# Kernel tuning notes

Measured on AMD Instinct MI355X. Metric: run time of the kernel, lower is better.

## Reference

```python
import jax, jax.numpy as jnp
import numpy as np

N_NODES = 100000
HID = 128
N_LAYERS = 3
N_EDGES = 1600000
EPS = 1e-5


def setup_inputs() -> dict:
    key = jax.random.key(0)
    ks = jax.random.split(key, 10)
    H, L = HID, N_LAYERS
    # edge_index: row 0 = src, row 1 = dst (PyG source_to_target flow)
    edge_index = jax.random.randint(ks[0], (2, N_EDGES), 0, N_NODES, dtype=jnp.int32)
    # xavier-uniform embedding
    lim = float(np.sqrt(6.0 / (N_NODES + H)))
    emb = jax.random.uniform(ks[1], (N_NODES, H), jnp.float32, -lim, lim)
    s = 1.0 / np.sqrt(H)
    Wl = jax.random.uniform(ks[2], (L, H, H), jnp.float32, -s, s)  # lin_l (neighbors), has bias
    bl = jax.random.uniform(ks[3], (L, H), jnp.float32, -s, s)
    Wr = jax.random.uniform(ks[4], (L, H, H), jnp.float32, -s, s)  # lin_r (root), no bias
    ln_gamma = jnp.ones((L, H), jnp.float32)
    ln_beta = jnp.zeros((L, H), jnp.float32)
    sj = 1.0 / np.sqrt(H * (L + 1))
    jkW = jax.random.uniform(ks[5], (H, H * (L + 1)), jnp.float32, -sj, sj)
    jkb = jax.random.uniform(ks[6], (H,), jnp.float32, -sj, sj)
    return {"emb": emb, "Wl": Wl, "bl": bl, "Wr": Wr,
            "ln_gamma": ln_gamma, "ln_beta": ln_beta,
            "jkW": jkW, "jkb": jkb, "edge_index": edge_index}


def _layernorm(x, gamma, beta):
    mu = jnp.mean(x, axis=-1, keepdims=True)
    var = jnp.mean(jnp.square(x - mu), axis=-1, keepdims=True)
    return (x - mu) * jax.lax.rsqrt(var + EPS) * gamma + beta


def reference(emb, Wl, bl, Wr, ln_gamma, ln_beta, jkW, jkb, edge_index):
    src, dst = edge_index[0], edge_index[1]
    n = emb.shape[0]
    # in-degree for mean aggregation (clamped to avoid div-by-zero)
    deg = jax.ops.segment_sum(jnp.ones_like(dst, dtype=emb.dtype), dst, num_segments=n)
    inv_deg = (1.0 / jnp.maximum(deg, 1.0))[:, None]
    x = emb
    xs = [x]
    for i in range(N_LAYERS):
        x_prev = x
        # scatter-mean of neighbor features (gather [E,H] -> segment_sum [N,H])
        agg = jax.ops.segment_sum(x[src], dst, num_segments=n) * inv_deg
        # SAGEConv: lin_l(agg) + lin_r(x)
        x = agg @ Wl[i].T + bl[i] + x @ Wr[i].T
        x = _layernorm(x, ln_gamma[i], ln_beta[i])
        x = jax.nn.relu(x)
        # dropout is identity in eval mode
        if i > 0:
            x = x + x_prev
        xs.append(x)
    # jumping-knowledge concat + projection
    x = jnp.concatenate(xs, axis=1) @ jkW.T + jkb
    return x
```

## Files before the change

kernel.cpp:

```cpp
#include <hip/hip_runtime.h>
#include <hip/hip_bf16.h>
#include <stdint.h>

#define HID 128

typedef __attribute__((ext_vector_type(8))) __bf16 bf16x8;
typedef __attribute__((ext_vector_type(4))) float f32x4;

static __device__ __forceinline__ float bf2f(ushort h){
  union { uint u; float f; } c; c.u = ((uint)h) << 16; return c.f;
}
static __device__ __forceinline__ ushort f2bf(float f){
  union { float f; uint u; } c; c.f = f;
  uint u = c.u;
  return (ushort)((u + 0x7fffu + ((u >> 16) & 1u)) >> 16);
}
static __device__ __forceinline__ bf16x8 load8(const ushort* p){
  return *(const bf16x8*)p;
}

__global__ void k_cvt(const float* __restrict__ in, ushort* __restrict__ out, int n){
  int i = blockIdx.x * 256 + threadIdx.x;
  if (i < n) out[i] = f2bf(in[i]);
}

__global__ void k_cvtw(const float* __restrict__ Wl, const float* __restrict__ Wr,
                       ushort* __restrict__ outF, int total){
  int o = blockIdx.x * 256 + threadIdx.x;
  if (o >= total) return;
  int layer = o >> 15;
  int r = o & 32767;
  int e    = r & 7;
  int lane = (r >> 3) & 63;
  int jt   = (r >> 9) & 7;
  int mat  = (r >> 12) & 1;
  int kt   = r >> 13;
  int l16 = lane & 15, quad = lane >> 4;
  int j = jt * 16 + l16;
  int k = kt * 32 + quad * 8 + e;
  const float* W = mat ? Wr : Wl;
  outF[o] = f2bf(W[layer * 16384 + j * 128 + k]);
}

__global__ void k_cvtjk(const float* __restrict__ jkW, ushort* __restrict__ outF){
  int o = blockIdx.x * 256 + threadIdx.x;
  int e    = o & 7;
  int lane = (o >> 3) & 63;
  int jt   = (o >> 9) & 7;
  int kt   = o >> 12;
  int l16 = lane & 15, quad = lane >> 4;
  int j = jt * 16 + l16;
  int k = kt * 32 + quad * 8 + e;
  outF[o] = f2bf(jkW[j * 512 + k]);
}

__global__ void k_hist(const int* __restrict__ dst, int* __restrict__ cnt, int E){
  int e = blockIdx.x * 256 + threadIdx.x;
  if (e < E) atomicAdd(&cnt[dst[e]], 1);
}

__global__ void k_scan1(const int* __restrict__ cnt, int* __restrict__ offs,
                        int* __restrict__ bsums, int n){
  int gid = blockIdx.x * 1024 + threadIdx.x;
  int v = (gid < n) ? cnt[gid] : 0;
  int lane = threadIdx.x & 63, w = threadIdx.x >> 6;
  int x = v;
  #pragma unroll
  for (int d = 1; d < 64; d <<= 1){ int y = __shfl_up(x, d, 64); if (lane >= d) x += y; }
  __shared__ int tmp[16];
  if (lane == 63) tmp[w] = x;
  __syncthreads();
  if (threadIdx.x < 64){
    int s = (lane < 16) ? tmp[lane] : 0;
    #pragma unroll
    for (int d = 1; d < 16; d <<= 1){ int y = __shfl_up(s, d, 64); if (lane >= d) s += y; }
    if (lane < 16) tmp[lane] = s;
  }
  __syncthreads();
  int base = (w > 0) ? tmp[w - 1] : 0;
  int incl = base + x;
  if (gid < n) offs[gid] = incl - v;
  if (threadIdx.x == 1023) bsums[blockIdx.x] = incl;
}

__global__ void k_scan2(int* bsums, int nb){
  if (threadIdx.x == 0 && blockIdx.x == 0){
    int acc = 0;
    for (int i = 0; i < nb; i++){ int v = bsums[i]; bsums[i] = acc; acc += v; }
  }
}

__global__ void k_scan3(int* __restrict__ offs, const int* __restrict__ bsums, int n){
  int gid = blockIdx.x * 1024 + threadIdx.x;
  if (gid < n) offs[gid] += bsums[blockIdx.x];
}

__global__ void k_bucket(const int* __restrict__ src, const int* __restrict__ dst,
                         const int* __restrict__ offs, int* __restrict__ cursor,
                         int* __restrict__ csr, int E){
  int e = blockIdx.x * 256 + threadIdx.x;
  if (e < E){
    int d = dst[e];
    int p = atomicAdd(&cursor[d], 1);
    csr[offs[d] + p] = src[e];
  }
}

__global__ __launch_bounds__(256) void k_aggregate(
    const ushort* __restrict__ x, const int* __restrict__ csr,
    const int* __restrict__ offs, const int* __restrict__ cnt,
    ushort* __restrict__ agg, int N){
  int node = blockIdx.x * 4 + (threadIdx.x >> 6);
  int lane = threadIdx.x & 63;
  if (node >= N) return;
  int beg = offs[node], d = cnt[node];
  const int* __restrict__ cp = csr + beg;
  float s0 = 0.f, s1 = 0.f;
  int i = 0;
  for (; i + 8 <= d; i += 8){
    int idx[8];
    #pragma unroll
    for (int u = 0; u < 8; u++) idx[u] = cp[i + u];
    uint v[8];
    #pragma unroll
    for (int u = 0; u < 8; u++)
      v[u] = *(const uint*)(x + (size_t)idx[u] * HID + lane * 2);
    #pragma unroll
    for (int u = 0; u < 8; u++){
      s0 += bf2f((ushort)v[u]);
      s1 += bf2f((ushort)(v[u] >> 16));
    }
  }
  if (i + 4 <= d){
    int idx[4];
    #pragma unroll
    for (int u = 0; u < 4; u++) idx[u] = cp[i + u];
    uint v[4];
    #pragma unroll
    for (int u = 0; u < 4; u++)
      v[u] = *(const uint*)(x + (size_t)idx[u] * HID + lane * 2);
    #pragma unroll
    for (int u = 0; u < 4; u++){
      s0 += bf2f((ushort)v[u]);
      s1 += bf2f((ushort)(v[u] >> 16));
    }
    i += 4;
  }
  for (; i < d; i++){
    int s = cp[i];
    uint v = *(const uint*)(x + (size_t)s * HID + lane * 2);
    s0 += bf2f((ushort)v);
    s1 += bf2f((ushort)(v >> 16));
  }
  float inv = 1.0f / fmaxf((float)d, 1.0f);
  uint o = (uint)f2bf(s0 * inv) | ((uint)f2bf(s1 * inv) << 16);
  *(uint*)(agg + (size_t)node * HID + lane * 2) = o;
}

template<int HAS_RES>
__global__ __launch_bounds__(256) void k_layer(
    const ushort* __restrict__ agg, const ushort* __restrict__ xin,
    const ushort* __restrict__ Wf,
    const float* __restrict__ bl, const float* __restrict__ gamma,
    const float* __restrict__ beta,
    ushort* __restrict__ xout, int N){
  __shared__ ushort sB[8192];
  int tid = threadIdx.x;
  int wv = tid >> 6, lane = tid & 63;
  int quad = lane >> 4, l16 = lane & 15;
  int rowbase = blockIdx.x * 128 + wv * 32;
  int r0 = rowbase + l16;      if (r0 >= N) r0 = N - 1;
  int r1 = rowbase + 16 + l16; if (r1 >= N) r1 = N - 1;

  f32x4 acc[2][8];
  #pragma unroll
  for (int jt = 0; jt < 8; jt++){
    float b = bl[jt * 16 + l16];
    f32x4 c = {b, b, b, b};
    acc[0][jt] = c; acc[1][jt] = c;
  }

  #pragma unroll
  for (int kt = 0; kt < 4; kt++){
    int ao = kt * 32 + quad * 8;
    bf16x8 a10 = load8(agg + (size_t)r0 * HID + ao);
    bf16x8 a11 = load8(agg + (size_t)r1 * HID + ao);
    bf16x8 a20 = load8(xin + (size_t)r0 * HID + ao);
    bf16x8 a21 = load8(xin + (size_t)r1 * HID + ao);
    __syncthreads();
    const ushort* src = Wf + kt * 8192;
    #pragma unroll
    for (int i = 0; i < 4; i++){
      int c = i * 256 + tid;
      *(bf16x8*)(sB + c * 8) = load8(src + c * 8);
    }
    __syncthreads();
    #pragma unroll
    for (int jt = 0; jt < 8; jt++){
      bf16x8 bL = load8(sB + (jt * 64 + lane) * 8);
      bf16x8 bR = load8(sB + ((8 + jt) * 64 + lane) * 8);
      acc[0][jt] = __builtin_amdgcn_mfma_f32_16x16x32_bf16(a10, bL, acc[0][jt], 0, 0, 0);
      acc[1][jt] = __builtin_amdgcn_mfma_f32_16x16x32_bf16(a11, bL, acc[1][jt], 0, 0, 0);
      acc[0][jt] = __builtin_amdgcn_mfma_f32_16x16x32_bf16(a20, bR, acc[0][jt], 0, 0, 0);
      acc[1][jt] = __builtin_amdgcn_mfma_f32_16x16x32_bf16(a21, bR, acc[1][jt], 0, 0, 0);
    }
  }

  #pragma unroll
  for (int rt = 0; rt < 2; rt++){
    float s1[4] = {0,0,0,0}, s2[4] = {0,0,0,0};
    #pragma unroll
    for (int jt = 0; jt < 8; jt++){
      #pragma unroll
      for (int r = 0; r < 4; r++){ float v = acc[rt][jt][r]; s1[r] += v; s2[r] += v * v; }
    }
    #pragma unroll
    for (int m = 1; m < 16; m <<= 1){
      #pragma unroll
      for (int r = 0; r < 4; r++){
        s1[r] += __shfl_xor(s1[r], m, 64);
        s2[r] += __shfl_xor(s2[r], m, 64);
      }
    }
    float mu[4], rs[4];
    #pragma unroll
    for (int r = 0; r < 4; r++){
      mu[r] = s1[r] * (1.f / 128.f);
      float var = s2[r] * (1.f / 128.f) - mu[r] * mu[r];
      rs[r] = rsqrtf(var + 1e-5f);
    }
    #pragma unroll
    for (int jt = 0; jt < 8; jt++){
      int col = jt * 16 + l16;
      float g = gamma[col], bb = beta[col];
      #pragma unroll
      for (int r = 0; r < 4; r++){
        int row = rowbase + rt * 16 + quad * 4 + r;
        if (row < N){
          float v = (acc[rt][jt][r] - mu[r]) * rs[r] * g + bb;
          v = fmaxf(v, 0.f);
          if (HAS_RES) v += bf2f(xin[(size_t)row * HID + col]);
          xout[(size_t)row * HID + col] = f2bf(v);
        }
      }
    }
  }
}

__global__ __launch_bounds__(256) void k_jk(
    const ushort* __restrict__ emb, const ushort* __restrict__ x1,
    const ushort* __restrict__ x2, const ushort* __restrict__ x3,
    const ushort* __restrict__ Wf,
    const float* __restrict__ jkb, float* __restrict__ out, int N){
  __shared__ ushort sB[8192];
  int tid = threadIdx.x;
  int wv = tid >> 6, lane = tid & 63;
  int quad = lane >> 4, l16 = lane & 15;
  int rowbase = blockIdx.x * 128 + wv * 32;
  int r0 = rowbase + l16;      if (r0 >= N) r0 = N - 1;
  int r1 = rowbase + 16 + l16; if (r1 >= N) r1 = N - 1;

  f32x4 acc[2][8];
  #pragma unroll
  for (int jt = 0; jt < 8; jt++){
    float b = jkb[jt * 16 + l16];
    f32x4 c = {b, b, b, b};
    acc[0][jt] = c; acc[1][jt] = c;
  }

  const ushort* srcs[4] = {emb, x1, x2, x3};
  #pragma unroll
  for (int st = 0; st < 8; st++){
    int kt0 = st * 2, kt1 = st * 2 + 1;
    const ushort* sp0 = srcs[kt0 >> 2];
    const ushort* sp1 = srcs[kt1 >> 2];
    int ao0 = (kt0 & 3) * 32 + quad * 8;
    int ao1 = (kt1 & 3) * 32 + quad * 8;
    bf16x8 aA0 = load8(sp0 + (size_t)r0 * HID + ao0);
    bf16x8 aA1 = load8(sp0 + (size_t)r1 * HID + ao0);
    bf16x8 aB0 = load8(sp1 + (size_t)r0 * HID + ao1);
    bf16x8 aB1 = load8(sp1 + (size_t)r1 * HID + ao1);
    __syncthreads();
    const ushort* src = Wf + st * 8192;
    #pragma unroll
    for (int i = 0; i < 4; i++){
      int c = i * 256 + tid;
      *(bf16x8*)(sB + c * 8) = load8(src + c * 8);
    }
    __syncthreads();
    #pragma unroll
    for (int jt = 0; jt < 8; jt++){
      bf16x8 b0 = load8(sB + (jt * 64 + lane) * 8);
      bf16x8 b1 = load8(sB + ((8 + jt) * 64 + lane) * 8);
      acc[0][jt] = __builtin_amdgcn_mfma_f32_16x16x32_bf16(aA0, b0, acc[0][jt], 0, 0, 0);
      acc[1][jt] = __builtin_amdgcn_mfma_f32_16x16x32_bf16(aA1, b0, acc[1][jt], 0, 0, 0);
      acc[0][jt] = __builtin_amdgcn_mfma_f32_16x16x32_bf16(aB0, b1, acc[0][jt], 0, 0, 0);
      acc[1][jt] = __builtin_amdgcn_mfma_f32_16x16x32_bf16(aB1, b1, acc[1][jt], 0, 0, 0);
    }
  }

  #pragma unroll
  for (int rt = 0; rt < 2; rt++){
    #pragma unroll
    for (int jt = 0; jt < 8; jt++){
      #pragma unroll
      for (int r = 0; r < 4; r++){
        int row = rowbase + rt * 16 + quad * 4 + r;
        if (row < N)
          out[(size_t)row * HID + jt * 16 + l16] = acc[rt][jt][r];
      }
    }
  }
}

extern "C" void kernel_launch(void* const* d_in, const int* in_sizes, int n_in,
                              void* d_out, int out_size, void* d_ws, size_t ws_size,
                              hipStream_t stream){
  const float* emb   = (const float*)d_in[0];
  const float* Wl    = (const float*)d_in[1];
  const float* bl    = (const float*)d_in[2];
  const float* Wr    = (const float*)d_in[3];
  const float* gamma = (const float*)d_in[4];
  const float* beta  = (const float*)d_in[5];
  const float* jkW   = (const float*)d_in[6];
  const float* jkb   = (const float*)d_in[7];
  const int*   eidx  = (const int*)d_in[8];
  int N = in_sizes[0] / HID;
  int E = in_sizes[8] / 2;
  const int* src = eidx;
  const int* dst = eidx + E;
  float* out = (float*)d_out;

  char* w = (char*)d_ws;
  auto carve = [&](size_t bytes) -> char* {
    char* p = w; w += (bytes + 255) & ~(size_t)255; return p;
  };
  int Npad = ((N + 127) / 128) * 128;
  int* cnt      = (int*)carve((size_t)N * 4);
  int* offs     = (int*)carve((size_t)(N + 1) * 4);
  int* bsums    = (int*)carve(1024 * 4);
  int* cursor   = (int*)carve((size_t)N * 4);
  int* csr      = (int*)carve((size_t)E * 4);
  ushort* Wfrag = (ushort*)carve((size_t)3 * 32768 * 2);
  ushort* jkWf  = (ushort*)carve((size_t)65536 * 2);
  ushort* embbf = (ushort*)carve((size_t)Npad * HID * 2);
  ushort* agg   = (ushort*)carve((size_t)Npad * HID * 2);
  ushort* x1    = (ushort*)carve((size_t)Npad * HID * 2);
  ushort* x2    = (ushort*)carve((size_t)Npad * HID * 2);
  ushort* x3    = (ushort*)carve((size_t)Npad * HID * 2);

  hipMemsetAsync(cnt, 0, (size_t)N * 4, stream);
  hipMemsetAsync(cursor, 0, (size_t)N * 4, stream);

  int nEmb = N * HID;
  k_cvtw<<<(3 * 32768 + 255) / 256, 256, 0, stream>>>(Wl, Wr, Wfrag, 3 * 32768);
  k_cvtjk<<<65536 / 256, 256, 0, stream>>>(jkW, jkWf);
  k_cvt<<<(nEmb + 255) / 256, 256, 0, stream>>>(emb, embbf, nEmb);

  k_hist<<<(E + 255) / 256, 256, 0, stream>>>(dst, cnt, E);
  int nb = (N + 1023) / 1024;
  k_scan1<<<nb, 1024, 0, stream>>>(cnt, offs, bsums, N);
  k_scan2<<<1, 64, 0, stream>>>(bsums, nb);
  k_scan3<<<nb, 1024, 0, stream>>>(offs, bsums, N);
  k_bucket<<<(E + 255) / 256, 256, 0, stream>>>(src, dst, offs, cursor, csr, E);

  int aggBlocks = (N + 3) / 4;
  int gemmBlocks = (N + 127) / 128;

  k_aggregate<<<aggBlocks, 256, 0, stream>>>(embbf, csr, offs, cnt, agg, N);
  k_layer<0><<<gemmBlocks, 256, 0, stream>>>(agg, embbf, Wfrag, bl, gamma, beta, x1, N);
  k_aggregate<<<aggBlocks, 256, 0, stream>>>(x1, csr, offs, cnt, agg, N);
  k_layer<1><<<gemmBlocks, 256, 0, stream>>>(agg, x1, Wfrag + 32768, bl + HID,
                                             gamma + HID, beta + HID, x2, N);
  k_aggregate<<<aggBlocks, 256, 0, stream>>>(x2, csr, offs, cnt, agg, N);
  k_layer<1><<<gemmBlocks, 256, 0, stream>>>(agg, x2, Wfrag + 2 * 32768, bl + 2 * HID,
                                             gamma + 2 * HID, beta + 2 * HID, x3, N);
  k_jk<<<gemmBlocks, 256, 0, stream>>>(embbf, x1, x2, x3, jkWf, jkb, out, N);
}
```

Baseline: 631.5 us.

## Build CSR via coarse 128-node binning plus per-bin shared-memory counting sort

Replaces the global per-node histogram, three-kernel scan and atomic bucket scatter with three kernels. The first bins edges into 128-node buckets, packing source and local destination into one word. The second is a single-block scan over bucket counts. The third does a per-bucket counting sort in shared memory that writes offs, cnt and csr. This aims to cut kernel launches, memsets and scattered global atomics on per-node cursors. In exchange, all edges now hit a few hundred heavily contended bucket counters, and edges past the fixed 3072-per-bucket capacity are silently dropped. The single-block scan also caps the node count at about 131K.

```diff
diff --git a/kernel.cpp b/kernel.cpp
--- a/kernel.cpp
+++ b/kernel.cpp
@@ -3,6 +3,8 @@
 #include <stdint.h>
 
 #define HID 128
+#define BSHIFT 7
+#define BCAP 3072
 
 typedef __attribute__((ext_vector_type(8))) __bf16 bf16x8;
 typedef __attribute__((ext_vector_type(4))) float f32x4;
@@ -54,23 +56,29 @@
   outF[o] = f2bf(jkW[j * 512 + k]);
 }
 
-__global__ void k_hist(const int* __restrict__ dst, int* __restrict__ cnt, int E){
+__global__ void k_bin(const int* __restrict__ src, const int* __restrict__ dst,
+                      int* __restrict__ bcnt, uint* __restrict__ binned, int E){
   int e = blockIdx.x * 256 + threadIdx.x;
-  if (e < E) atomicAdd(&cnt[dst[e]], 1);
-}
-
-__global__ void k_scan1(const int* __restrict__ cnt, int* __restrict__ offs,
-                        int* __restrict__ bsums, int n){
-  int gid = blockIdx.x * 1024 + threadIdx.x;
-  int v = (gid < n) ? cnt[gid] : 0;
-  int lane = threadIdx.x & 63, w = threadIdx.x >> 6;
+  if (e < E){
+    int d = dst[e];
+    int b = d >> BSHIFT;
+    int pos = atomicAdd(&bcnt[b], 1);
+    if (pos < BCAP)
+      binned[(size_t)b * BCAP + pos] = ((uint)src[e] << BSHIFT) | (uint)(d & 127);
+  }
+}
+
+__global__ void k_bscan(const int* __restrict__ bcnt, int* __restrict__ bbase, int nb){
+  int tid = threadIdx.x;
+  int v = (tid < nb) ? min(bcnt[tid], BCAP) : 0;
+  int lane = tid & 63, w = tid >> 6;
   int x = v;
   #pragma unroll
   for (int d = 1; d < 64; d <<= 1){ int y = __shfl_up(x, d, 64); if (lane >= d) x += y; }
   __shared__ int tmp[16];
   if (lane == 63) tmp[w] = x;
   __syncthreads();
-  if (threadIdx.x < 64){
+  if (tid < 64){
     int s = (lane < 16) ? tmp[lane] : 0;
     #pragma unroll
     for (int d = 1; d < 16; d <<= 1){ int y = __shfl_up(s, d, 64); if (lane >= d) s += y; }
@@ -78,31 +86,55 @@
   }
   __syncthreads();
   int base = (w > 0) ? tmp[w - 1] : 0;
-  int incl = base + x;
-  if (gid < n) offs[gid] = incl - v;
-  if (threadIdx.x == 1023) bsums[blockIdx.x] = incl;
-}
-
-__global__ void k_scan2(int* bsums, int nb){
-  if (threadIdx.x == 0 && blockIdx.x == 0){
-    int acc = 0;
-    for (int i = 0; i < nb; i++){ int v = bsums[i]; bsums[i] = acc; acc += v; }
-  }
-}
-
-__global__ void k_scan3(int* __restrict__ offs, const int* __restrict__ bsums, int n){
-  int gid = blockIdx.x * 1024 + threadIdx.x;
-  if (gid < n) offs[gid] += bsums[blockIdx.x];
-}
-
-__global__ void k_bucket(const int* __restrict__ src, const int* __restrict__ dst,
-                         const int* __restrict__ offs, int* __restrict__ cursor,
-                         int* __restrict__ csr, int E){
-  int e = blockIdx.x * 256 + threadIdx.x;
-  if (e < E){
-    int d = dst[e];
-    int p = atomicAdd(&cursor[d], 1);
-    csr[offs[d] + p] = src[e];
+  if (tid < nb) bbase[tid] = base + x - v;
+}
+
+__global__ __launch_bounds__(256) void k_bpass(
+    const uint* __restrict__ binned, const int* __restrict__ bcnt,
+    const int* __restrict__ bbase, int* __restrict__ csr,
+    int* __restrict__ offs, int* __restrict__ cnt, int N){
+  int b = blockIdx.x;
+  int n0 = b << BSHIFT;
+  int tid = threadIdx.x;
+  __shared__ int lcnt[128], loffs[128];
+  if (tid < 128) lcnt[tid] = 0;
+  __syncthreads();
+  int m = min(bcnt[b], BCAP);
+  const uint* bp = binned + (size_t)b * BCAP;
+  uint vv[12]; int slot[12];
+  #pragma unroll
+  for (int u = 0; u < 12; u++){
+    int i = tid + u * 256;
+    if (i < m){
+      uint v = bp[i];
+      vv[u] = v;
+      slot[u] = atomicAdd(&lcnt[v & 127], 1);
+    }
+  }
+  __syncthreads();
+  if (tid < 64){
+    int a0 = lcnt[tid * 2], a1 = lcnt[tid * 2 + 1];
+    int s = a0 + a1;
+    int x = s;
+    #pragma unroll
+    for (int d = 1; d < 64; d <<= 1){ int y = __shfl_up(x, d, 64); if (tid >= d) x += y; }
+    int excl = x - s;
+    loffs[tid * 2] = excl;
+    loffs[tid * 2 + 1] = excl + a0;
+  }
+  __syncthreads();
+  int base = bbase[b];
+  if (tid < 128 && n0 + tid < N){
+    cnt[n0 + tid] = lcnt[tid];
+    offs[n0 + tid] = base + loffs[tid];
+  }
+  #pragma unroll
+  for (int u = 0; u < 12; u++){
+    int i = tid + u * 256;
+    if (i < m){
+      uint v = vv[u];
+      csr[base + loffs[v & 127] + slot[u]] = (int)(v >> BSHIFT);
+    }
   }
 }
 
@@ -331,15 +363,18 @@
   const int* dst = eidx + E;
   float* out = (float*)d_out;
 
+  int NB = (N + 127) >> BSHIFT;
+
   char* w = (char*)d_ws;
   auto carve = [&](size_t bytes) -> char* {
     char* p = w; w += (bytes + 255) & ~(size_t)255; return p;
   };
   int Npad = ((N + 127) / 128) * 128;
+  int* bcnt     = (int*)carve((size_t)NB * 4);
+  int* bbase    = (int*)carve((size_t)NB * 4);
+  uint* binned  = (uint*)carve((size_t)NB * BCAP * 4);
   int* cnt      = (int*)carve((size_t)N * 4);
-  int* offs     = (int*)carve((size_t)(N + 1) * 4);
-  int* bsums    = (int*)carve(1024 * 4);
-  int* cursor   = (int*)carve((size_t)N * 4);
+  int* offs     = (int*)carve((size_t)N * 4);
   int* csr      = (int*)carve((size_t)E * 4);
   ushort* Wfrag = (ushort*)carve((size_t)3 * 32768 * 2);
   ushort* jkWf  = (ushort*)carve((size_t)65536 * 2);
@@ -349,20 +384,16 @@
   ushort* x2    = (ushort*)carve((size_t)Npad * HID * 2);
   ushort* x3    = (ushort*)carve((size_t)Npad * HID * 2);
 
-  hipMemsetAsync(cnt, 0, (size_t)N * 4, stream);
-  hipMemsetAsync(cursor, 0, (size_t)N * 4, stream);
+  hipMemsetAsync(bcnt, 0, (size_t)NB * 4, stream);
 
   int nEmb = N * HID;
   k_cvtw<<<(3 * 32768 + 255) / 256, 256, 0, stream>>>(Wl, Wr, Wfrag, 3 * 32768);
   k_cvtjk<<<65536 / 256, 256, 0, stream>>>(jkW, jkWf);
   k_cvt<<<(nEmb + 255) / 256, 256, 0, stream>>>(emb, embbf, nEmb);
 
-  k_hist<<<(E + 255) / 256, 256, 0, stream>>>(dst, cnt, E);
-  int nb = (N + 1023) / 1024;
-  k_scan1<<<nb, 1024, 0, stream>>>(cnt, offs, bsums, N);
-  k_scan2<<<1, 64, 0, stream>>>(bsums, nb);
-  k_scan3<<<nb, 1024, 0, stream>>>(offs, bsums, N);
-  k_bucket<<<(E + 255) / 256, 256, 0, stream>>>(src, dst, offs, cursor, csr, E);
+  k_bin<<<(E + 255) / 256, 256, 0, stream>>>(src, dst, bcnt, binned, E);
+  k_bscan<<<1, 1024, 0, stream>>>(bcnt, bbase, NB);
+  k_bpass<<<NB, 256, 0, stream>>>(binned, bcnt, bbase, csr, offs, cnt, N);
 
   int aggBlocks = (N + 3) / 4;
   int gemmBlocks = (N + 127) / 128;
```

Measured after the change: 865.2 us. 1.37x slower.
